# Kernel tuning notes

Hardware: AMD Instinct MI355X
Metric: run time of the kernel (lower is better)

## Reference

```python
import math
import jax, jax.numpy as jnp
import numpy as np

HEADS = 8
DIM = 512
HEAD_SIZE = DIM // HEADS  # 64


def setup_inputs() -> dict:
    key = jax.random.key(0)
    ks = jax.random.split(key, 5)
    b, nh, nw, t, d = 16, 16, 16, 16, DIM
    x = jax.random.normal(ks[0], (b, nh, nw, t, d), dtype=jnp.float32)
    s = 1.0 / math.sqrt(d)
    Wq = jax.random.normal(ks[1], (d, d), dtype=jnp.float32) * s
    Wk = jax.random.normal(ks[2], (d, d), dtype=jnp.float32) * s
    Wv = jax.random.normal(ks[3], (d, d), dtype=jnp.float32) * s
    Wo = jax.random.normal(ks[4], (d, d), dtype=jnp.float32) * s
    z = jnp.zeros((d,), dtype=jnp.float32)
    return {"x": x, "Wq": Wq, "bq": z, "Wk": Wk, "bk": z, "Wv": Wv, "bv": z, "Wo": Wo, "bo": z}


def _split_heads(t):
    # [b, n1, n2, T, D] -> [b, n1, n2, H, T, hs]
    b, n1, n2, T, _ = t.shape
    return t.reshape(b, n1, n2, T, HEADS, HEAD_SIZE).transpose(0, 1, 2, 4, 3, 5)


def reference(x, Wq, bq, Wk, bk, Wv, bv, Wo, bo):
    q = _split_heads(x @ Wq + bq)
    k = _split_heads(x @ Wk + bk)
    v = _split_heads(x @ Wv + bv)
    # windowed attention scores: [b, n1, n2, H, T, T]
    scores = jnp.einsum('bnmhtd,bnmhsd->bnmhts', q, k) / math.sqrt(HEAD_SIZE)
    probs = jax.nn.sigmoid(scores)  # NOTE: elementwise sigmoid, not softmax
    ctx = jnp.einsum('bnmhts,bnmhsd->bnmhtd', probs, v)
    b, n1, n2, H, T, hs = ctx.shape
    ctx = ctx.transpose(0, 1, 2, 4, 3, 5).reshape(b, n1, n2, T, H * hs)
    return ctx @ Wo + bo
```

## Files before the change

### kernel.cpp

```cpp
#include <hip/hip_runtime.h>
#include <hip/hip_bf16.h>

typedef float f32x4 __attribute__((ext_vector_type(4)));
typedef __bf16 bf16x8 __attribute__((ext_vector_type(8)));
typedef __bf16 bf16x4 __attribute__((ext_vector_type(4)));
typedef unsigned short u16x4 __attribute__((ext_vector_type(4)));
typedef unsigned short u16x8 __attribute__((ext_vector_type(8)));

__device__ __forceinline__ unsigned short f2bf(float f) {
  union { float f; unsigned u; } x; x.f = f;
  unsigned r = x.u + 0x7FFFu + ((x.u >> 16) & 1u);
  return (unsigned short)(r >> 16);
}
__device__ __forceinline__ float bf2f(unsigned short u) {
  union { unsigned u; float f; } x; x.u = ((unsigned)u) << 16;
  return x.f;
}

__device__ __forceinline__ void gl16(const void* g, void* l) {
  __builtin_amdgcn_global_load_lds(
      (const __attribute__((address_space(1))) unsigned*)g,
      (__attribute__((address_space(3))) unsigned*)l, 16, 0, 0);
}

__global__ __launch_bounds__(256) void prep_wt(const float* __restrict__ Wq,
                                               const float* __restrict__ Wk,
                                               const float* __restrict__ Wv,
                                               const float* __restrict__ Wo,
                                               unsigned short* __restrict__ WT) {
  __shared__ unsigned short ts[64][65];
  const float* W = (blockIdx.z == 0) ? Wq : (blockIdx.z == 1) ? Wk
                   : (blockIdx.z == 2) ? Wv : Wo;
  const int t = threadIdx.x;
  const int kbase = blockIdx.y * 64;
  const int nbase = blockIdx.x * 64;
  for (int i = 0; i < 16; ++i) {
    int idx = i * 256 + t;
    int r = idx >> 6, c = idx & 63;
    ts[r][c] = f2bf(W[(size_t)(kbase + r) * 512 + nbase + c]);
  }
  __syncthreads();
  unsigned short* dst = WT + (size_t)blockIdx.z * 512 * 512;
  for (int i = 0; i < 16; ++i) {
    int idx = i * 256 + t;
    int nn = idx >> 6, kk = idx & 63;
    dst[(size_t)(nbase + nn) * 512 + kbase + kk] = ts[kk][nn];
  }
}

__global__ void prep_bias(const float* __restrict__ bq, const float* __restrict__ bk,
                          const float* __restrict__ bv, float* __restrict__ biasc) {
  int i = blockIdx.x * 256 + threadIdx.x;
  if (i < 512) biasc[i] = bq[i];
  else if (i < 1024) biasc[i] = bk[i - 512];
  else if (i < 1536) biasc[i] = bv[i - 1024];
}

template <typename AT, typename CT>
__global__ __launch_bounds__(512, 2) void gemm256(
    const AT* __restrict__ A, int lda,
    const unsigned short* __restrict__ BT,
    CT* __restrict__ C, int ldc,
    const float* __restrict__ bias, int NB) {
  __shared__ alignas(16) unsigned short pool[65536];
  const int t = threadIdx.x;
  const int lane = t & 63;
  const int w = t >> 6;
  const int wm = w >> 2, wn = w & 3;

  const int nwg = gridDim.x;
  const int cpx = nwg >> 3;
  const int wg = (blockIdx.x & 7) * cpx + (blockIdx.x >> 3);
  const int n0 = (wg % NB) * 256;
  const int m0 = (wg / NB) * 256;

  const int sr = lane >> 3;
  const int sg = ((lane & 7) ^ sr) << 3;
  const unsigned short* gB = BT + (size_t)(n0 + w * 8 + sr) * 512 + sg;
  const int lw = w * 512;

#define SB(kt, h, b)                                                        \
  { const unsigned short* g_ = gB + (size_t)(h) * 128 * 512 + (kt) * 64;    \
    unsigned short* l_ = &pool[32768 + (b) * 16384 + (h) * 8192 + lw];      \
    gl16(g_, l_); gl16(g_ + (size_t)64 * 512, l_ + 4096); }

  const unsigned short* gAu = nullptr;
  if constexpr (sizeof(AT) == 2)
    gAu = (const unsigned short*)A + (size_t)(m0 + w * 8 + sr) * lda + sg;
#define SA(kt, h, b)                                                        \
  { const unsigned short* g_ = gAu + (size_t)(h) * 128 * lda + (kt) * 64;   \
    unsigned short* l_ = &pool[(b) * 16384 + (h) * 8192 + lw];              \
    gl16(g_, l_); gl16(g_ + (size_t)64 * lda, l_ + 4096); }

  f32x4 ar[4][2];
  const int seg = t & 7;
  const int rbase = t >> 3;
  const float* gAf = nullptr;
  if constexpr (sizeof(AT) == 4)
    gAf = (const float*)A + (size_t)(m0 + rbase) * lda + seg * 8;
#define LA(kt, u)                                                           \
  { const float* g_ = gAf + (size_t)(u) * 64 * lda + (kt) * 64;             \
    ar[u][0] = *reinterpret_cast<const f32x4*>(g_);                         \
    ar[u][1] = *reinterpret_cast<const f32x4*>(g_ + 4); }
#define WA(u, b)                                                            \
  { int row_ = rbase + (u) * 64;                                            \
    bf16x8 pk_;                                                             \
    _Pragma("unroll") for (int j_ = 0; j_ < 4; ++j_) {                      \
      pk_[j_] = (__bf16)ar[u][0][j_];                                       \
      pk_[4 + j_] = (__bf16)ar[u][1][j_];                                   \
    }                                                                       \
    *reinterpret_cast<bf16x8*>(                                             \
        &pool[(b) * 16384 + row_ * 64 + ((seg ^ (row_ & 7)) << 3)]) = pk_; }

  const int fr = lane & 15;
  const int fg = lane >> 4;
  const int fx = lane & 7;
  auto readA = [&](int b, int mi, int kf) -> bf16x8 {
    return *reinterpret_cast<const bf16x8*>(
        &pool[(b) * 16384 + (wm * 128 + mi * 16 + fr) * 64 +
              ((((kf << 2) + fg) ^ fx) << 3)]);
  };
  auto readB = [&](int b, int ni, int kf) -> bf16x8 {
    return *reinterpret_cast<const bf16x8*>(
        &pool[32768 + (b) * 16384 + (wn * 64 + ni * 16 + fr) * 64 +
              ((((kf << 2) + fg) ^ fx) << 3)]);
  };

  f32x4 acc[8][4];
#pragma unroll
  for (int i = 0; i < 8; ++i)
#pragma unroll
    for (int j = 0; j < 4; ++j) acc[i][j] = (f32x4){0.f, 0.f, 0.f, 0.f};
  bf16x8 bfr[4][2];

#define PHASE(b, q, READB, STAGES, VM)                                       \
  {                                                                          \
    bf16x8 a0_ = readA(b, 2 * (q), 0), a1_ = readA(b, 2 * (q), 1);           \
    bf16x8 a2_ = readA(b, 2 * (q) + 1, 0), a3_ = readA(b, 2 * (q) + 1, 1);   \
    if (READB) {                                                             \
      _Pragma("unroll") for (int ni = 0; ni < 4; ++ni) {                     \
        bfr[ni][0] = readB(b, ni, 0);                                        \
        bfr[ni][1] = readB(b, ni, 1);                                        \
      }                                                                      \
    }                                                                        \
    STAGES;                                                                  \
    if ((VM) == 4) asm volatile("s_waitcnt vmcnt(4)" ::: "memory");          \
    if ((VM) == 0) asm volatile("s_waitcnt vmcnt(0)" ::: "memory");          \
    __builtin_amdgcn_s_barrier();                                            \
    asm volatile("s_waitcnt lgkmcnt(0)" ::: "memory");                       \
    __builtin_amdgcn_sched_barrier(0);                                       \
    __builtin_amdgcn_s_setprio(1);                                           \
    _Pragma("unroll") for (int ni = 0; ni < 4; ++ni) {                       \
      acc[2 * (q)][ni] = __builtin_amdgcn_mfma_f32_16x16x32_bf16(            \
          bfr[ni][0], a0_, acc[2 * (q)][ni], 0, 0, 0);                       \
      acc[2 * (q) + 1][ni] = __builtin_amdgcn_mfma_f32_16x16x32_bf16(        \
          bfr[ni][0], a2_, acc[2 * (q) + 1][ni], 0, 0, 0);                   \
    }                                                                        \
    _Pragma("unroll") for (int ni = 0; ni < 4; ++ni) {                       \
      acc[2 * (q)][ni] = __builtin_amdgcn_mfma_f32_16x16x32_bf16(            \
          bfr[ni][1], a1_, acc[2 * (q)][ni], 0, 0, 0);                       \
      acc[2 * (q) + 1][ni] = __builtin_amdgcn_mfma_f32_16x16x32_bf16(        \
          bfr[ni][1], a3_, acc[2 * (q) + 1][ni], 0, 0, 0);                   \
    }                                                                        \
    __builtin_amdgcn_s_setprio(0);                                           \
    __builtin_amdgcn_s_barrier();                                            \
  }

  if constexpr (sizeof(AT) == 4) {
    LA(0, 0) LA(0, 1) LA(0, 2) LA(0, 3)
    SB(0, 0, 0) SB(0, 1, 0) SB(1, 0, 1) SB(1, 1, 1)
    WA(0, 0) WA(1, 0) WA(2, 0) WA(3, 0)
    asm volatile("s_waitcnt vmcnt(4) lgkmcnt(0)" ::: "memory");
    __builtin_amdgcn_s_barrier();
#pragma unroll
    for (int i = 0; i < 4; ++i) {
      const bool s2 = (i < 3);
      PHASE(0, 0, true,  { LA(2 * i + 1, 0) LA(2 * i + 1, 1) }, -1);
      PHASE(0, 1, false, { LA(2 * i + 1, 2) LA(2 * i + 1, 3) if (s2) SB(2 * i + 2, 0, 0) }, -1);
      PHASE(0, 2, false, { WA(0, 1) WA(1, 1) if (s2) SB(2 * i + 2, 1, 0) }, -1);
      PHASE(0, 3, false, { WA(2, 1) WA(3, 1) }, s2 ? 4 : 0);
      PHASE(1, 0, true,  { if (s2) { LA(2 * i + 2, 0) LA(2 * i + 2, 1) } }, -1);
      PHASE(1, 1, false, { if (s2) { LA(2 * i + 2, 2) LA(2 * i + 2, 3) SB(2 * i + 3, 0, 1) } }, -1);
      PHASE(1, 2, false, { if (s2) { WA(0, 0) WA(1, 0) SB(2 * i + 3, 1, 1) } }, -1);
      PHASE(1, 3, false, { if (s2) { WA(2, 0) WA(3, 0) } }, s2 ? 4 : 0);
    }
  } else {
    SB(0, 0, 0) SB(0, 1, 0)
    SA(0, 0, 0) SA(0, 1, 0)
    SB(1, 0, 1) SB(1, 1, 1)
    asm volatile("s_waitcnt vmcnt(4)" ::: "memory");
    __builtin_amdgcn_s_barrier();
#pragma unroll
    for (int i = 0; i < 4; ++i) {
      const bool s2 = (i < 3);
      PHASE(0, 0, true,  { SA(2 * i + 1, 0, 1) }, -1);
      PHASE(0, 1, false, { SA(2 * i + 1, 1, 1) if (s2) SB(2 * i + 2, 0, 0) }, -1);
      PHASE(0, 2, false, { if (s2) SB(2 * i + 2, 1, 0) }, -1);
      PHASE(0, 3, false, {}, s2 ? 4 : 0);
      PHASE(1, 0, true,  { if (s2) SA(2 * i + 2, 0, 0) }, -1);
      PHASE(1, 1, false, { if (s2) SA(2 * i + 2, 1, 0) }, -1);
      PHASE(1, 2, false, { if (s2) SB(2 * i + 3, 0, 1) }, -1);
      PHASE(1, 3, false, { if (s2) SB(2 * i + 3, 1, 1) }, s2 ? 4 : 0);
    }
  }
#undef PHASE
#undef SA
#undef SB
#undef LA
#undef WA

#pragma unroll
  for (int mi = 0; mi < 8; ++mi) {
    const size_t m = (size_t)(m0 + wm * 128 + mi * 16 + fr);
#pragma unroll
    for (int ni = 0; ni < 4; ++ni) {
      const int nb = n0 + wn * 64 + ni * 16 + fg * 4;
      f32x4 b4 = *reinterpret_cast<const f32x4*>(&bias[nb]);
      if constexpr (sizeof(CT) == 2) {
        u16x4 o;
#pragma unroll
        for (int r = 0; r < 4; ++r) o[r] = f2bf(acc[mi][ni][r] + b4[r]);
        *reinterpret_cast<u16x4*>(&C[m * ldc + nb]) = o;
      } else {
        f32x4 o = acc[mi][ni] + b4;
        *reinterpret_cast<f32x4*>(&C[m * ldc + nb]) = o;
      }
    }
  }
}

__global__ __launch_bounds__(256) void attn_kernel(unsigned short* __restrict__ QKV) {
  __shared__ alignas(16) unsigned short qs[16][1544];
  __shared__ unsigned short ps[8][16][16];
  const int t = threadIdx.x;
  const size_t base = (size_t)blockIdx.x * 16;

  {
    int row = t >> 4;
    int cb = (t & 15) * 96;
    const unsigned short* src = QKV + (base + row) * 1536;
#pragma unroll
    for (int i = 0; i < 24; ++i) {
      int c = cb + i * 4;
      *reinterpret_cast<u16x4*>(&qs[row][c]) = *reinterpret_cast<const u16x4*>(&src[c]);
    }
  }
  __syncthreads();

  const int tq = t >> 4;
  const int tk = t & 15;
#pragma unroll
  for (int h = 0; h < 8; ++h) {
    float acc = 0.f;
#pragma unroll
    for (int dc = 0; dc < 64; dc += 8) {
      u16x8 q8 = *reinterpret_cast<const u16x8*>(&qs[tq][h * 64 + dc]);
      u16x8 k8 = *reinterpret_cast<const u16x8*>(&qs[tk][512 + h * 64 + dc]);
#pragma unroll
      for (int j = 0; j < 8; ++j) acc += bf2f(q8[j]) * bf2f(k8[j]);
    }
    ps[h][tq][tk] = f2bf(1.0f / (1.0f + __expf(-acc * 0.125f)));
  }
  __syncthreads();

  const int row = t >> 4;
  const int cb4 = (t & 15) * 4;
  unsigned short* dst = QKV + (base + row) * 1536 + 1024;
#pragma unroll
  for (int h = 0; h < 8; ++h) {
    f32x4 acc = (f32x4){0.f, 0.f, 0.f, 0.f};
#pragma unroll
    for (int s = 0; s < 16; ++s) {
      float p = bf2f(ps[h][row][s]);
      u16x4 v4 = *reinterpret_cast<const u16x4*>(&qs[s][1024 + h * 64 + cb4]);
      acc[0] += p * bf2f(v4[0]); acc[1] += p * bf2f(v4[1]);
      acc[2] += p * bf2f(v4[2]); acc[3] += p * bf2f(v4[3]);
    }
    u16x4 o4;
    o4[0] = f2bf(acc[0]); o4[1] = f2bf(acc[1]); o4[2] = f2bf(acc[2]); o4[3] = f2bf(acc[3]);
    *reinterpret_cast<u16x4*>(&dst[h * 64 + cb4]) = o4;
  }
}

extern "C" void kernel_launch(void* const* d_in, const int* in_sizes, int n_in,
                              void* d_out, int out_size, void* d_ws, size_t ws_size,
                              hipStream_t stream) {
  const float* x  = (const float*)d_in[0];
  const float* Wq = (const float*)d_in[1];
  const float* bq = (const float*)d_in[2];
  const float* Wk = (const float*)d_in[3];
  const float* bk = (const float*)d_in[4];
  const float* Wv = (const float*)d_in[5];
  const float* bv = (const float*)d_in[6];
  const float* Wo = (const float*)d_in[7];
  const float* bo = (const float*)d_in[8];
  float* out = (float*)d_out;

  const int M = 65536;
  char* ws = (char*)d_ws;
  unsigned short* WT = (unsigned short*)ws;
  float* biasc = (float*)(ws + (size_t)2048 * 512 * 2);
  const long long prep_bytes = (long long)2048 * 512 * 2 + 8192;

  prep_wt<<<dim3(8, 8, 4), 256, 0, stream>>>(Wq, Wk, Wv, Wo, WT);
  prep_bias<<<6, 256, 0, stream>>>(bq, bk, bv, biasc);

  long long avail = (long long)ws_size - prep_bytes;
  int chunk_rows = 65536;
  while (chunk_rows > 2048 && (long long)chunk_rows * 3072 > avail) chunk_rows >>= 1;
  const int nchunks = M / chunk_rows;

  unsigned short* QKV = (unsigned short*)(ws + prep_bytes);

  for (int c = 0; c < nchunks; ++c) {
    const size_t row0 = (size_t)c * chunk_rows;
    const int mt = chunk_rows / 256;
    gemm256<float, unsigned short><<<mt * 6, 512, 0, stream>>>(
        x + row0 * 512, 512, WT, QKV, 1536, biasc, 6);
    attn_kernel<<<chunk_rows / 16, 256, 0, stream>>>(QKV);
    gemm256<unsigned short, float><<<mt * 2, 512, 0, stream>>>(
        QKV + 1024, 1536, WT + (size_t)1536 * 512, out + row0 * 512, 512, bo, 2);
  }
}
```

Measured before the change: 327.0 us.

## Pre-convert x to bf16 and compute windowed attention with MFMA

Adds a separate pass that converts x to bf16, so the QKV GEMM loads A directly through the async global-to-LDS path instead of converting fp32 in registers inside the pipeline. The scalar per-thread attention kernel is replaced by one that runs QK^T and PV on 16x16x32 bf16 MFMAs, handling 8 windows per block and looping over heads with swizzled LDS staging. The cost is an extra full read and write of x plus a larger workspace footprint, and the attention kernel now syncs once per head.

```diff
diff --git a/kernel.cpp b/kernel.cpp
--- a/kernel.cpp
+++ b/kernel.cpp
@@ -3,7 +3,6 @@
 
 typedef float f32x4 __attribute__((ext_vector_type(4)));
 typedef __bf16 bf16x8 __attribute__((ext_vector_type(8)));
-typedef __bf16 bf16x4 __attribute__((ext_vector_type(4)));
 typedef unsigned short u16x4 __attribute__((ext_vector_type(4)));
 typedef unsigned short u16x8 __attribute__((ext_vector_type(8)));
 
@@ -11,10 +10,6 @@
   union { float f; unsigned u; } x; x.f = f;
   unsigned r = x.u + 0x7FFFu + ((x.u >> 16) & 1u);
   return (unsigned short)(r >> 16);
-}
-__device__ __forceinline__ float bf2f(unsigned short u) {
-  union { unsigned u; float f; } x; x.u = ((unsigned)u) << 16;
-  return x.f;
 }
 
 __device__ __forceinline__ void gl16(const void* g, void* l) {
@@ -56,9 +51,24 @@
   else if (i < 1536) biasc[i] = bv[i - 1024];
 }
 
-template <typename AT, typename CT>
+__global__ __launch_bounds__(256) void convert_x(const float* __restrict__ x,
+                                                 unsigned short* __restrict__ xb,
+                                                 long long n8) {
+  long long i = (long long)blockIdx.x * 256 + threadIdx.x;
+  const long long stride = (long long)gridDim.x * 256;
+  for (; i < n8; i += stride) {
+    f32x4 a = *reinterpret_cast<const f32x4*>(&x[i * 8]);
+    f32x4 b = *reinterpret_cast<const f32x4*>(&x[i * 8 + 4]);
+    u16x8 o;
+    o[0] = f2bf(a[0]); o[1] = f2bf(a[1]); o[2] = f2bf(a[2]); o[3] = f2bf(a[3]);
+    o[4] = f2bf(b[0]); o[5] = f2bf(b[1]); o[6] = f2bf(b[2]); o[7] = f2bf(b[3]);
+    *reinterpret_cast<u16x8*>(&xb[i * 8]) = o;
+  }
+}
+
+template <typename CT>
 __global__ __launch_bounds__(512, 2) void gemm256(
-    const AT* __restrict__ A, int lda,
+    const unsigned short* __restrict__ A, int lda,
     const unsigned short* __restrict__ BT,
     CT* __restrict__ C, int ldc,
     const float* __restrict__ bias, int NB) {
@@ -76,41 +86,18 @@
 
   const int sr = lane >> 3;
   const int sg = ((lane & 7) ^ sr) << 3;
+  const unsigned short* gA = A + (size_t)(m0 + w * 8 + sr) * lda + sg;
   const unsigned short* gB = BT + (size_t)(n0 + w * 8 + sr) * 512 + sg;
   const int lw = w * 512;
 
+#define SA(kt, h, b)                                                        \
+  { const unsigned short* g_ = gA + (size_t)(h) * 128 * lda + (kt) * 64;    \
+    unsigned short* l_ = &pool[(b) * 16384 + (h) * 8192 + lw];              \
+    gl16(g_, l_); gl16(g_ + (size_t)64 * lda, l_ + 4096); }
 #define SB(kt, h, b)                                                        \
   { const unsigned short* g_ = gB + (size_t)(h) * 128 * 512 + (kt) * 64;    \
     unsigned short* l_ = &pool[32768 + (b) * 16384 + (h) * 8192 + lw];      \
     gl16(g_, l_); gl16(g_ + (size_t)64 * 512, l_ + 4096); }
-
-  const unsigned short* gAu = nullptr;
-  if constexpr (sizeof(AT) == 2)
-    gAu = (const unsigned short*)A + (size_t)(m0 + w * 8 + sr) * lda + sg;
-#define SA(kt, h, b)                                                        \
-  { const unsigned short* g_ = gAu + (size_t)(h) * 128 * lda + (kt) * 64;   \
-    unsigned short* l_ = &pool[(b) * 16384 + (h) * 8192 + lw];              \
-    gl16(g_, l_); gl16(g_ + (size_t)64 * lda, l_ + 4096); }
-
-  f32x4 ar[4][2];
-  const int seg = t & 7;
-  const int rbase = t >> 3;
-  const float* gAf = nullptr;
-  if constexpr (sizeof(AT) == 4)
-    gAf = (const float*)A + (size_t)(m0 + rbase) * lda + seg * 8;
-#define LA(kt, u)                                                           \
-  { const float* g_ = gAf + (size_t)(u) * 64 * lda + (kt) * 64;             \
-    ar[u][0] = *reinterpret_cast<const f32x4*>(g_);                         \
-    ar[u][1] = *reinterpret_cast<const f32x4*>(g_ + 4); }
-#define WA(u, b)                                                            \
-  { int row_ = rbase + (u) * 64;                                            \
-    bf16x8 pk_;                                                             \
-    _Pragma("unroll") for (int j_ = 0; j_ < 4; ++j_) {                      \
-      pk_[j_] = (__bf16)ar[u][0][j_];                                       \
-      pk_[4 + j_] = (__bf16)ar[u][1][j_];                                   \
-    }                                                                       \
-    *reinterpret_cast<bf16x8*>(                                             \
-        &pool[(b) * 16384 + row_ * 64 + ((seg ^ (row_ & 7)) << 3)]) = pk_; }
 
   const int fr = lane & 15;
   const int fg = lane >> 4;
@@ -166,48 +153,27 @@
     __builtin_amdgcn_s_barrier();                                            \
   }
 
-  if constexpr (sizeof(AT) == 4) {
-    LA(0, 0) LA(0, 1) LA(0, 2) LA(0, 3)
-    SB(0, 0, 0) SB(0, 1, 0) SB(1, 0, 1) SB(1, 1, 1)
-    WA(0, 0) WA(1, 0) WA(2, 0) WA(3, 0)
-    asm volatile("s_waitcnt vmcnt(4) lgkmcnt(0)" ::: "memory");
-    __builtin_amdgcn_s_barrier();
-#pragma unroll
-    for (int i = 0; i < 4; ++i) {
-      const bool s2 = (i < 3);
-      PHASE(0, 0, true,  { LA(2 * i + 1, 0) LA(2 * i + 1, 1) }, -1);
-      PHASE(0, 1, false, { LA(2 * i + 1, 2) LA(2 * i + 1, 3) if (s2) SB(2 * i + 2, 0, 0) }, -1);
-      PHASE(0, 2, false, { WA(0, 1) WA(1, 1) if (s2) SB(2 * i + 2, 1, 0) }, -1);
-      PHASE(0, 3, false, { WA(2, 1) WA(3, 1) }, s2 ? 4 : 0);
-      PHASE(1, 0, true,  { if (s2) { LA(2 * i + 2, 0) LA(2 * i + 2, 1) } }, -1);
-      PHASE(1, 1, false, { if (s2) { LA(2 * i + 2, 2) LA(2 * i + 2, 3) SB(2 * i + 3, 0, 1) } }, -1);
-      PHASE(1, 2, false, { if (s2) { WA(0, 0) WA(1, 0) SB(2 * i + 3, 1, 1) } }, -1);
-      PHASE(1, 3, false, { if (s2) { WA(2, 0) WA(3, 0) } }, s2 ? 4 : 0);
-    }
-  } else {
-    SB(0, 0, 0) SB(0, 1, 0)
-    SA(0, 0, 0) SA(0, 1, 0)
-    SB(1, 0, 1) SB(1, 1, 1)
-    asm volatile("s_waitcnt vmcnt(4)" ::: "memory");
-    __builtin_amdgcn_s_barrier();
-#pragma unroll
-    for (int i = 0; i < 4; ++i) {
-      const bool s2 = (i < 3);
-      PHASE(0, 0, true,  { SA(2 * i + 1, 0, 1) }, -1);
-      PHASE(0, 1, false, { SA(2 * i + 1, 1, 1) if (s2) SB(2 * i + 2, 0, 0) }, -1);
-      PHASE(0, 2, false, { if (s2) SB(2 * i + 2, 1, 0) }, -1);
-      PHASE(0, 3, false, {}, s2 ? 4 : 0);
-      PHASE(1, 0, true,  { if (s2) SA(2 * i + 2, 0, 0) }, -1);
-      PHASE(1, 1, false, { if (s2) SA(2 * i + 2, 1, 0) }, -1);
-      PHASE(1, 2, false, { if (s2) SB(2 * i + 3, 0, 1) }, -1);
-      PHASE(1, 3, false, { if (s2) SB(2 * i + 3, 1, 1) }, s2 ? 4 : 0);
-    }
+  SB(0, 0, 0) SB(0, 1, 0)
+  SA(0, 0, 0) SA(0, 1, 0)
+  SB(1, 0, 1) SB(1, 1, 1)
+  asm volatile("s_waitcnt vmcnt(4)" ::: "memory");
+  __builtin_amdgcn_s_barrier();
+
+#pragma unroll
+  for (int i = 0; i < 4; ++i) {
+    const bool s2 = (i < 3);
+    PHASE(0, 0, true,  { SA(2 * i + 1, 0, 1) }, -1);
+    PHASE(0, 1, false, { SA(2 * i + 1, 1, 1) if (s2) SB(2 * i + 2, 0, 0) }, -1);
+    PHASE(0, 2, false, { if (s2) SB(2 * i + 2, 1, 0) }, -1);
+    PHASE(0, 3, false, {}, s2 ? 4 : 0);
+    PHASE(1, 0, true,  { if (s2) SA(2 * i + 2, 0, 0) }, -1);
+    PHASE(1, 1, false, { if (s2) SA(2 * i + 2, 1, 0) }, -1);
+    PHASE(1, 2, false, { if (s2) SB(2 * i + 3, 0, 1) }, -1);
+    PHASE(1, 3, false, { if (s2) SB(2 * i + 3, 1, 1) }, s2 ? 4 : 0);
   }
 #undef PHASE
 #undef SA
 #undef SB
-#undef LA
-#undef WA
 
 #pragma unroll
   for (int mi = 0; mi < 8; ++mi) {
@@ -229,56 +195,70 @@
   }
 }
 
-__global__ __launch_bounds__(256) void attn_kernel(unsigned short* __restrict__ QKV) {
-  __shared__ alignas(16) unsigned short qs[16][1544];
-  __shared__ unsigned short ps[8][16][16];
+__global__ __launch_bounds__(256) void attn_mfma(unsigned short* __restrict__ QKV) {
+  __shared__ alignas(16) unsigned short sh[24576];
+  __shared__ alignas(16) unsigned short ps[1024];
   const int t = threadIdx.x;
-  const size_t base = (size_t)blockIdx.x * 16;
-
-  {
-    int row = t >> 4;
-    int cb = (t & 15) * 96;
-    const unsigned short* src = QKV + (base + row) * 1536;
-#pragma unroll
-    for (int i = 0; i < 24; ++i) {
-      int c = cb + i * 4;
-      *reinterpret_cast<u16x4*>(&qs[row][c]) = *reinterpret_cast<const u16x4*>(&src[c]);
+  const int lane = t & 63;
+  const int w = t >> 6;
+  const int fr = lane & 15, fg = lane >> 4, fx = lane & 7;
+  const size_t base = (size_t)blockIdx.x * 128;
+  const int srw = lane >> 3;
+  const int sgq = lane & 7;
+
+  for (int h = 0; h < 8; ++h) {
+#pragma unroll
+    for (int i = 0; i < 4; ++i) {
+      const int c = i * 4 + w;
+      const int win = c >> 1;
+      const int row = (c & 1) * 8 + srw;
+      const unsigned short* srow =
+          QKV + (base + win * 16 + row) * 1536 + h * 64;
+      const int gsw = (sgq ^ (row & 7)) << 3;
+      gl16(srow + gsw,               &sh[c * 512]);
+      gl16(srow + 512 + gsw,         &sh[8192 + c * 512]);
+      gl16(srow + 1024 + (sgq << 3), &sh[16384 + c * 512]);
     }
-  }
-  __syncthreads();
-
-  const int tq = t >> 4;
-  const int tk = t & 15;
-#pragma unroll
-  for (int h = 0; h < 8; ++h) {
-    float acc = 0.f;
-#pragma unroll
-    for (int dc = 0; dc < 64; dc += 8) {
-      u16x8 q8 = *reinterpret_cast<const u16x8*>(&qs[tq][h * 64 + dc]);
-      u16x8 k8 = *reinterpret_cast<const u16x8*>(&qs[tk][512 + h * 64 + dc]);
-#pragma unroll
-      for (int j = 0; j < 8; ++j) acc += bf2f(q8[j]) * bf2f(k8[j]);
+    asm volatile("s_waitcnt vmcnt(0)" ::: "memory");
+    __syncthreads();
+#pragma unroll
+    for (int ww = 0; ww < 2; ++ww) {
+      const int wi = w * 2 + ww;
+      const int qb = wi * 1024;
+      f32x4 s = (f32x4){0.f, 0.f, 0.f, 0.f};
+#pragma unroll
+      for (int kk = 0; kk < 2; ++kk) {
+        const int go = ((((kk << 2) + fg) ^ fx) << 3);
+        bf16x8 kf = *reinterpret_cast<const bf16x8*>(&sh[8192 + qb + fr * 64 + go]);
+        bf16x8 qf = *reinterpret_cast<const bf16x8*>(&sh[qb + fr * 64 + go]);
+        s = __builtin_amdgcn_mfma_f32_16x16x32_bf16(kf, qf, s, 0, 0, 0);
+      }
+      u16x4 pfu;
+#pragma unroll
+      for (int r = 0; r < 4; ++r)
+        pfu[r] = f2bf(1.0f / (1.0f + __expf(-s[r] * 0.125f)));
+      *reinterpret_cast<u16x4*>(&ps[w * 256 + fr * 16 + fg * 4]) = pfu;
+      u16x8 pbu = (u16x8){0, 0, 0, 0, 0, 0, 0, 0};
+      if (fg < 2)
+        pbu = *reinterpret_cast<const u16x8*>(&ps[w * 256 + fr * 16 + fg * 8]);
+      bf16x8 pb = __builtin_bit_cast(bf16x8, pbu);
+#pragma unroll
+      for (int dc = 0; dc < 4; ++dc) {
+        u16x8 vau;
+#pragma unroll
+        for (int j = 0; j < 8; ++j)
+          vau[j] = sh[16384 + qb + ((fg & 1) * 8 + j) * 64 + dc * 16 + fr];
+        bf16x8 va = __builtin_bit_cast(bf16x8, vau);
+        f32x4 c = __builtin_amdgcn_mfma_f32_16x16x32_bf16(
+            va, pb, (f32x4){0.f, 0.f, 0.f, 0.f}, 0, 0, 0);
+        u16x4 o;
+#pragma unroll
+        for (int r = 0; r < 4; ++r) o[r] = f2bf(c[r]);
+        *reinterpret_cast<u16x4*>(
+            &QKV[(base + wi * 16 + fr) * 1536 + 1024 + h * 64 + dc * 16 + fg * 4]) = o;
+      }
     }
-    ps[h][tq][tk] = f2bf(1.0f / (1.0f + __expf(-acc * 0.125f)));
-  }
-  __syncthreads();
-
-  const int row = t >> 4;
-  const int cb4 = (t & 15) * 4;
-  unsigned short* dst = QKV + (base + row) * 1536 + 1024;
-#pragma unroll
-  for (int h = 0; h < 8; ++h) {
-    f32x4 acc = (f32x4){0.f, 0.f, 0.f, 0.f};
-#pragma unroll
-    for (int s = 0; s < 16; ++s) {
-      float p = bf2f(ps[h][row][s]);
-      u16x4 v4 = *reinterpret_cast<const u16x4*>(&qs[s][1024 + h * 64 + cb4]);
-      acc[0] += p * bf2f(v4[0]); acc[1] += p * bf2f(v4[1]);
-      acc[2] += p * bf2f(v4[2]); acc[3] += p * bf2f(v4[3]);
-    }
-    u16x4 o4;
-    o4[0] = f2bf(acc[0]); o4[1] = f2bf(acc[1]); o4[2] = f2bf(acc[2]); o4[3] = f2bf(acc[3]);
-    *reinterpret_cast<u16x4*>(&dst[h * 64 + cb4]) = o4;
+    __syncthreads();
   }
 }
 
@@ -307,18 +287,21 @@
 
   long long avail = (long long)ws_size - prep_bytes;
   int chunk_rows = 65536;
-  while (chunk_rows > 2048 && (long long)chunk_rows * 3072 > avail) chunk_rows >>= 1;
+  while (chunk_rows > 2048 && (long long)chunk_rows * 4096 > avail) chunk_rows >>= 1;
   const int nchunks = M / chunk_rows;
 
-  unsigned short* QKV = (unsigned short*)(ws + prep_bytes);
+  unsigned short* Xb  = (unsigned short*)(ws + prep_bytes);
+  unsigned short* QKV = Xb + (size_t)chunk_rows * 512;
 
   for (int c = 0; c < nchunks; ++c) {
     const size_t row0 = (size_t)c * chunk_rows;
     const int mt = chunk_rows / 256;
-    gemm256<float, unsigned short><<<mt * 6, 512, 0, stream>>>(
-        x + row0 * 512, 512, WT, QKV, 1536, biasc, 6);
-    attn_kernel<<<chunk_rows / 16, 256, 0, stream>>>(QKV);
-    gemm256<unsigned short, float><<<mt * 2, 512, 0, stream>>>(
+    convert_x<<<2048, 256, 0, stream>>>(x + row0 * 512, Xb,
+                                        (long long)chunk_rows * 64);
+    gemm256<unsigned short><<<mt * 6, 512, 0, stream>>>(
+        Xb, 512, WT, QKV, 1536, biasc, 6);
+    attn_mfma<<<chunk_rows / 128, 256, 0, stream>>>(QKV);
+    gemm256<float><<<mt * 2, 512, 0, stream>>>(
         QKV + 1024, 1536, WT + (size_t)1536 * 512, out + row0 * 512, 512, bo, 2);
   }
 }
```

Result: faster. 304.5 us (-6.9%).
